# Optimization experiments

Measured on AMD Instinct MI355X. Metric: run time of the kernel, lower is better.

Reference implementation:

```python
import jax, jax.numpy as jnp
import numpy as np

B, L, A, S, H, K, M = 2048, 2, 4, 128, 256, 16, 131072


def _norm(x):
    # normalize_location: project onto unit sphere (last dim)
    return x / jnp.linalg.norm(x, axis=-1, keepdims=True)


def _mlp(x, W1, b1, W2, b2):
    return jax.nn.relu(x @ W1 + b1) @ W2 + b2


def _localizer_dist(loc, act, W1, b1, W2, b2, V1, c1, V2, c2, vs_logits):
    mean = _mlp(jnp.concatenate([loc, act], axis=1), W1, b1, W2, b2)
    sd = jnp.exp(_mlp(mean, V1, c1, V2, c2))
    sd = jnp.exp(vs_logits) * sd + 1e-6  # vs_logits has shape [L-1]==[1], broadcasts
    return mean, sd


def setup_inputs():
    key = jax.random.key(0)
    ks = jax.random.split(key, 12)
    return {
        'sensory': jax.random.normal(ks[0], (B, S)),
        'last_location': jax.random.normal(ks[1], (B, L)),
        'action': jax.random.normal(ks[2], (B, A)),
        'heading': jax.random.normal(ks[3], (B, A)),
        'mem_locations': jax.random.normal(ks[4], (M, L)),
        'mem_sensory': jax.random.normal(ks[5], (M, S)),
        'W1': jax.random.normal(ks[6], (L + A, H)) * 0.1,
        'b1': jnp.zeros((H,)),
        'W2': jax.random.normal(ks[7], (H, L)) * 0.1,
        'b2': jnp.zeros((L,)),
        'V1': jax.random.normal(ks[8], (L, H)) * 0.1,
        'c1': jnp.zeros((H,)),
        'V2': jax.random.normal(ks[9], (H, L)) * 0.1,
        'c2': jnp.zeros((L,)),
        'vs_logits': jnp.zeros((L - 1,)),
        'mem_valid_count': 8,
        'write_ptr': 1000,
    }


def reference(sensory, last_location, action, heading, mem_locations, mem_sensory,
              W1, b1, W2, b2, V1, c1, V2, c2, vs_logits, mem_valid_count, write_ptr):
    neg_inf = jnp.asarray(-jnp.inf, sensory.dtype)
    # --- memory.search: cosine-sim KNN over stored sensory keys ---
    q = _norm(sensory)                              # [B,S]
    keys = _norm(mem_sensory)                       # [M,S]
    scores_all = q @ keys.T                         # [B,M] big retrieval matmul
    valid = jnp.arange(M) < mem_valid_count         # [M]
    scores_all = jnp.where(valid[None, :], scores_all, neg_inf)
    scores, idx = jax.lax.top_k(scores_all, K)      # [B,K]
    location_guesses = mem_locations[idx]           # gather: [B,K,L]
    found = jnp.full((B,), min(mem_valid_count, K))
    # --- localizer: sample next agent location ---
    noise1 = jax.random.normal(jax.random.key(1), (B, L))
    noise2 = jax.random.normal(jax.random.key(2), (B, L))
    mean1, sd1 = _localizer_dist(last_location, action, W1, b1, W2, b2, V1, c1, V2, c2, vs_logits)
    next_location = mean1 + noise1 * sd1
    nl_lp = (-0.5 * (((next_location - mean1) / sd1) ** 2).sum(-1).mean()
             - jnp.log(sd1).sum(-1).mean())
    mean2, sd2 = _localizer_dist(next_location, heading, W1, b1, W2, b2, V1, c1, V2, c2, vs_logits)
    invalid_guess_mask = jnp.arange(K)[None, :] >= found[:, None]   # [B,K]
    ignore = found == 0                                             # [B]
    # --- select_location: masked similarity softmax over guesses ---
    # NOTE: torch `a.where(cond, b)` == where(cond, a, b); arg order preserved faithfully.
    matches = jnp.einsum('bkl,bl->bk', _norm(location_guesses), _norm(mean2))
    matches = jnp.where(invalid_guess_mask, matches, neg_inf)
    w = jax.nn.softmax(matches, axis=-1)
    integrated = jnp.einsum('bk,bkl->bl', w, location_guesses)
    too_far = jnp.linalg.norm(-0.5 * ((integrated - mean2) / sd2), axis=-1) > 2.0
    expected = mean2 + noise2 * sd2
    cond = too_far[:, None] | ignore[:, None] | jnp.isnan(integrated)
    obj_location = jnp.where(cond, integrated, expected)
    obj_lp = (-0.5 * (((obj_location - mean2) / sd2) ** 2).sum(-1).mean()
              - jnp.log(sd2).sum(-1).mean())
    # --- memory.write: scatter into ring buffer ---
    pos = (write_ptr + jnp.arange(B)) % M
    new_mem_loc = mem_locations.at[pos].set(obj_location)
    new_mem_sens = mem_sensory.at[pos].set(sensory)
    return next_location, nl_lp + obj_lp, new_mem_loc, new_mem_sens
```

## Files before the change

### kernel.cpp

```cpp
#include <hip/hip_runtime.h>
#include <stdint.h>

namespace {

constexpr int Bn = 2048;
constexpr int Kn = 16;
constexpr int Mn = 131072;

constexpr int O_NEXT   = 0;
constexpr int O_SCALAR = Bn * 2;
constexpr int O_LOC    = O_SCALAR + 1;
constexpr int O_SENS   = O_LOC + Mn * 2;

constexpr int NCOMPB = 512;
constexpr int NCOPY  = 2048;

constexpr int SENS_N = Mn * 128;
constexpr uint32_t RMASK = Mn - 1;
constexpr int NGI  = SENS_N / 4;
constexpr int TOTU = NGI + Mn;

typedef float f32x4   __attribute__((ext_vector_type(4)));
typedef float f32x4_u __attribute__((ext_vector_type(4), aligned(4)));

__device__ __forceinline__ uint32_t rotl32(uint32_t v, int d) {
  return (v << d) | (v >> (32 - d));
}
__device__ __forceinline__ void tfround(uint32_t& x0, uint32_t& x1, int r) {
  x0 += x1; x1 = rotl32(x1, r); x1 ^= x0;
}
__device__ __forceinline__ void threefry2x32(uint32_t k0, uint32_t k1,
                                             uint32_t c0, uint32_t c1,
                                             uint32_t& o0, uint32_t& o1) {
  const uint32_t ks2 = k0 ^ k1 ^ 0x1BD11BDAu;
  uint32_t x0 = c0 + k0, x1 = c1 + k1;
  tfround(x0, x1, 13); tfround(x0, x1, 15); tfround(x0, x1, 26); tfround(x0, x1, 6);
  x0 += k1;  x1 += ks2 + 1u;
  tfround(x0, x1, 17); tfround(x0, x1, 29); tfround(x0, x1, 16); tfround(x0, x1, 24);
  x0 += ks2; x1 += k0 + 2u;
  tfround(x0, x1, 13); tfround(x0, x1, 15); tfround(x0, x1, 26); tfround(x0, x1, 6);
  x0 += k0;  x1 += k1 + 3u;
  tfround(x0, x1, 17); tfround(x0, x1, 29); tfround(x0, x1, 16); tfround(x0, x1, 24);
  x0 += k1;  x1 += ks2 + 4u;
  tfround(x0, x1, 13); tfround(x0, x1, 15); tfround(x0, x1, 26); tfround(x0, x1, 6);
  o0 = x0 + ks2;
  o1 = x1 + k0 + 5u;
}

__device__ __forceinline__ float erfinv_xla(float x) {
  float w = -log1pf(-x * x);
  float p;
  if (w < 5.0f) {
    w -= 2.5f;
    p = 2.81022636e-08f;
    p = fmaf(p, w, 3.43273939e-07f);
    p = fmaf(p, w, -3.5233877e-06f);
    p = fmaf(p, w, -4.39150654e-06f);
    p = fmaf(p, w, 0.00021858087f);
    p = fmaf(p, w, -0.00125372503f);
    p = fmaf(p, w, -0.00417768164f);
    p = fmaf(p, w, 0.246640727f);
    p = fmaf(p, w, 1.50140941f);
  } else {
    w = sqrtf(w) - 3.0f;
    p = -0.000200214257f;
    p = fmaf(p, w, 0.000100950558f);
    p = fmaf(p, w, 0.00134934322f);
    p = fmaf(p, w, -0.00367342844f);
    p = fmaf(p, w, 0.00573950773f);
    p = fmaf(p, w, -0.0076224613f);
    p = fmaf(p, w, 0.00943887047f);
    p = fmaf(p, w, 1.00167406f);
    p = fmaf(p, w, 2.83297682f);
  }
  return p * x;
}
__device__ __forceinline__ float bits_to_normal(uint32_t bits) {
  const float lo = __int_as_float(0xBF7FFFFF);
  float f = __uint_as_float((bits >> 9) | 0x3F800000u) - 1.0f;
  float u = fmaxf(lo, f * 2.0f + lo);
  return 1.41421356237f * erfinv_xla(u);
}
__device__ __forceinline__ float noise_part(uint32_t key_lo, uint32_t i) {
  uint32_t o0, o1;
  threefry2x32(0u, key_lo, 0u, i, o0, o1);
  return bits_to_normal(o0 ^ o1);
}

__device__ __forceinline__ float wave_sum(float v) {
#pragma unroll
  for (int off = 32; off > 0; off >>= 1) v += __shfl_xor(v, off);
  return v;
}

__device__ __forceinline__ void localizer_wave(
    int lane,
    float x0, float x1, float x2, float x3, float x4, float x5,
    const float* __restrict__ W1, const float* __restrict__ b1,
    const float* __restrict__ W2, const float* __restrict__ b2,
    const float* __restrict__ V1, const float* __restrict__ c1,
    const float* __restrict__ V2, const float* __restrict__ c2,
    float vs_exp,
    float& m0, float& m1, float& sd0, float& sd1) {
  const int h = lane << 2;
  const float4 bb = *(const float4*)(b1 + h);
  const float4 w0 = *(const float4*)(W1 + h);
  const float4 w1 = *(const float4*)(W1 + 256 + h);
  const float4 w2 = *(const float4*)(W1 + 512 + h);
  const float4 w3 = *(const float4*)(W1 + 768 + h);
  const float4 w4 = *(const float4*)(W1 + 1024 + h);
  const float4 w5 = *(const float4*)(W1 + 1280 + h);
  float t0 = bb.x, t1 = bb.y, t2 = bb.z, t3 = bb.w;
  t0 = fmaf(x0, w0.x, t0); t1 = fmaf(x0, w0.y, t1); t2 = fmaf(x0, w0.z, t2); t3 = fmaf(x0, w0.w, t3);
  t0 = fmaf(x1, w1.x, t0); t1 = fmaf(x1, w1.y, t1); t2 = fmaf(x1, w1.z, t2); t3 = fmaf(x1, w1.w, t3);
  t0 = fmaf(x2, w2.x, t0); t1 = fmaf(x2, w2.y, t1); t2 = fmaf(x2, w2.z, t2); t3 = fmaf(x2, w2.w, t3);
  t0 = fmaf(x3, w3.x, t0); t1 = fmaf(x3, w3.y, t1); t2 = fmaf(x3, w3.z, t2); t3 = fmaf(x3, w3.w, t3);
  t0 = fmaf(x4, w4.x, t0); t1 = fmaf(x4, w4.y, t1); t2 = fmaf(x4, w4.z, t2); t3 = fmaf(x4, w4.w, t3);
  t0 = fmaf(x5, w5.x, t0); t1 = fmaf(x5, w5.y, t1); t2 = fmaf(x5, w5.z, t2); t3 = fmaf(x5, w5.w, t3);
  t0 = fmaxf(t0, 0.f); t1 = fmaxf(t1, 0.f); t2 = fmaxf(t2, 0.f); t3 = fmaxf(t3, 0.f);
  const float4 u0 = *(const float4*)(W2 + 2 * h);
  const float4 u1 = *(const float4*)(W2 + 2 * h + 4);
  float pa0 = t0 * u0.x; float pa1 = t0 * u0.y;
  pa0 = fmaf(t1, u0.z, pa0); pa1 = fmaf(t1, u0.w, pa1);
  pa0 = fmaf(t2, u1.x, pa0); pa1 = fmaf(t2, u1.y, pa1);
  pa0 = fmaf(t3, u1.z, pa0); pa1 = fmaf(t3, u1.w, pa1);
  m0 = wave_sum(pa0) + b2[0];
  m1 = wave_sum(pa1) + b2[1];

  const float4 cc = *(const float4*)(c1 + h);
  const float4 v0 = *(const float4*)(V1 + h);
  const float4 v1 = *(const float4*)(V1 + 256 + h);
  float s0 = cc.x, s1 = cc.y, s2 = cc.z, s3 = cc.w;
  s0 = fmaf(m0, v0.x, s0); s1 = fmaf(m0, v0.y, s1); s2 = fmaf(m0, v0.z, s2); s3 = fmaf(m0, v0.w, s3);
  s0 = fmaf(m1, v1.x, s0); s1 = fmaf(m1, v1.y, s1); s2 = fmaf(m1, v1.z, s2); s3 = fmaf(m1, v1.w, s3);
  s0 = fmaxf(s0, 0.f); s1 = fmaxf(s1, 0.f); s2 = fmaxf(s2, 0.f); s3 = fmaxf(s3, 0.f);
  const float4 q0 = *(const float4*)(V2 + 2 * h);
  const float4 q1 = *(const float4*)(V2 + 2 * h + 4);
  float ps0 = s0 * q0.x; float ps1 = s0 * q0.y;
  ps0 = fmaf(s1, q0.z, ps0); ps1 = fmaf(s1, q0.w, ps1);
  ps0 = fmaf(s2, q1.x, ps0); ps1 = fmaf(s2, q1.y, ps1);
  ps0 = fmaf(s3, q1.z, ps0); ps1 = fmaf(s3, q1.w, ps1);
  const float sv0 = wave_sum(ps0) + c2[0];
  const float sv1 = wave_sum(ps1) + c2[1];
  sd0 = fmaf(vs_exp, expf(sv0), 1e-6f);
  sd1 = fmaf(vs_exp, expf(sv1), 1e-6f);
}

__global__ __launch_bounds__(256) void fused_kernel(
    const float* __restrict__ sensory, const float* __restrict__ last_location,
    const float* __restrict__ action, const float* __restrict__ heading,
    const float* __restrict__ mem_locations, const float* __restrict__ mem_sensory,
    const float* __restrict__ W1, const float* __restrict__ b1,
    const float* __restrict__ W2, const float* __restrict__ b2,
    const float* __restrict__ V1, const float* __restrict__ c1,
    const float* __restrict__ V2, const float* __restrict__ c2,
    const float* __restrict__ vs_logits,
    const int* __restrict__ mvc_p, const int* __restrict__ wp_p,
    float* __restrict__ out, float* __restrict__ ws) {
  const int mvc = *mvc_p;
  const uint32_t wpm = (uint32_t)(*wp_p) & RMASK;

  if (blockIdx.x >= NCOMPB) {
    const int stride = NCOPY * 256;
    for (int u = (int)(blockIdx.x - NCOMPB) * 256 + (int)threadIdx.x;
         u < TOTU; u += stride) {
      if (u < NGI) {
        const uint32_t r  = (uint32_t)u >> 5;
        const uint32_t bb = (r - wpm) & RMASK;
        const int e = 4 * u;
        const float* src = (bb < Bn) ? (sensory + ((bb << 7) | (e & 127)))
                                     : (mem_sensory + e);
        const f32x4 q = *(const f32x4*)src;
        __builtin_nontemporal_store(q, (f32x4_u*)(out + O_SENS + e));
      } else {
        const uint32_t r = (uint32_t)(u - NGI);
        const uint32_t bb = (r - wpm) & RMASK;
        if (bb >= Bn) {
          const float2 v = *(const float2*)(mem_locations + 2 * r);
          out[O_LOC + 2 * r]     = v.x;
          out[O_LOC + 2 * r + 1] = v.y;
        }
      }
    }
  } else {
    __shared__ float redc[4][4];
    const int cb = blockIdx.x;
    const int wid = threadIdx.x >> 6;
    const int lane = threadIdx.x & 63;
    const int b = cb * 4 + wid;

    const uint32_t nk = 1u + ((lane >> 1) & 1u);
    const uint32_t ni = (uint32_t)(2 * b) + (lane & 1u);
    const float nv = noise_part(nk, ni);
    const float n1a = __shfl(nv, 0);
    const float n1b = __shfl(nv, 1);
    const float n2a = __shfl(nv, 2);
    const float n2b = __shfl(nv, 3);

    const float vs_exp = expf(vs_logits[0]);
    const float l0 = last_location[2 * b], l1 = last_location[2 * b + 1];
    const float a0 = action[4 * b],     a1 = action[4 * b + 1];
    const float a2 = action[4 * b + 2], a3 = action[4 * b + 3];
    const float h0 = heading[4 * b],     h1 = heading[4 * b + 1];
    const float h2 = heading[4 * b + 2], h3 = heading[4 * b + 3];

    float m10, m11, sd10, sd11;
    localizer_wave(lane, l0, l1, a0, a1, a2, a3, W1, b1, W2, b2, V1, c1, V2, c2,
                   vs_exp, m10, m11, sd10, sd11);
    const float nl0 = m10 + n1a * sd10;
    const float nl1 = m11 + n1b * sd11;
    if (lane == 0) *(float2*)(out + 2 * b) = make_float2(nl0, nl1);

    const float d0 = (nl0 - m10) / sd10;
    const float d1 = (nl1 - m11) / sd11;
    const float v_sq1 = d0 * d0 + d1 * d1;
    const float v_lg1 = logf(sd10) + logf(sd11);

    float m20, m21, sd20, sd21;
    localizer_wave(lane, nl0, nl1, h0, h1, h2, h3, W1, b1, W2, b2, V1, c1, V2, c2,
                   vs_exp, m20, m21, sd20, sd21);

    const int found = (mvc < Kn) ? mvc : Kn;
    const bool ignore = (found == 0);
    const float NEG_INF = -__builtin_huge_valf();

    const float qn = sqrtf(m20 * m20 + m21 * m21);
    const float q0 = m20 / qn, q1 = m21 / qn;

    float mk[Kn];
#pragma unroll
    for (int k = 0; k < Kn; ++k) {
      if (k >= found) {
        const float g0 = mem_locations[2 * k], g1 = mem_locations[2 * k + 1];
        const float gn = sqrtf(g0 * g0 + g1 * g1);
        mk[k] = (g0 / gn) * q0 + (g1 / gn) * q1;
      } else {
        mk[k] = NEG_INF;
      }
    }
    float mmax = NEG_INF;
#pragma unroll
    for (int k = 0; k < Kn; ++k) mmax = fmaxf(mmax, mk[k]);
    float wsum = 0.f;
#pragma unroll
    for (int k = 0; k < Kn; ++k) {
      mk[k] = expf(mk[k] - mmax);
      wsum += mk[k];
    }
    float i0 = 0.f, i1 = 0.f;
#pragma unroll
    for (int k = 0; k < Kn; ++k) {
      const float wn = mk[k] / wsum;
      i0 = fmaf(wn, mem_locations[2 * k], i0);
      i1 = fmaf(wn, mem_locations[2 * k + 1], i1);
    }

    const float z0 = (i0 - m20) / sd20, z1 = (i1 - m21) / sd21;
    const float hz0 = -0.5f * z0, hz1 = -0.5f * z1;
    const bool too_far = sqrtf(hz0 * hz0 + hz1 * hz1) > 2.0f;
    const float e0 = m20 + n2a * sd20;
    const float e1 = m21 + n2b * sd21;
    const bool c0 = too_far || ignore || __builtin_isnan(i0);
    const bool c1 = too_far || ignore || __builtin_isnan(i1);
    const float o0 = c0 ? i0 : e0;
    const float o1 = c1 ? i1 : e1;

    if (lane == 0) {
      const uint32_t row = (wpm + (uint32_t)b) & RMASK;
      out[O_LOC + 2 * row]     = o0;
      out[O_LOC + 2 * row + 1] = o1;
    }

    const float zo0 = (o0 - m20) / sd20, zo1 = (o1 - m21) / sd21;
    const float v_sq2 = zo0 * zo0 + zo1 * zo1;
    const float v_lg2 = logf(sd20) + logf(sd21);

    if (lane == 0) {
      redc[wid][0] = v_sq1; redc[wid][1] = v_lg1;
      redc[wid][2] = v_sq2; redc[wid][3] = v_lg2;
    }
    __syncthreads();
    if (threadIdx.x == 0) {
      float s0 = 0.f, s1 = 0.f, s2 = 0.f, s3 = 0.f;
#pragma unroll
      for (int w = 0; w < 4; ++w) {
        s0 += redc[w][0]; s1 += redc[w][1]; s2 += redc[w][2]; s3 += redc[w][3];
      }
      ws[4 * cb + 0] = s0; ws[4 * cb + 1] = s1;
      ws[4 * cb + 2] = s2; ws[4 * cb + 3] = s3;
    }
  }
}

__global__ void finalize_kernel(const float* __restrict__ ws, float* __restrict__ out) {
  const int lane = threadIdx.x;
  float s0 = 0.f, s1 = 0.f, s2 = 0.f, s3 = 0.f;
  for (int i = lane; i < NCOMPB; i += 64) {
    s0 += ws[4 * i + 0]; s1 += ws[4 * i + 1];
    s2 += ws[4 * i + 2]; s3 += ws[4 * i + 3];
  }
#pragma unroll
  for (int off = 32; off > 0; off >>= 1) {
    s0 += __shfl_xor(s0, off); s1 += __shfl_xor(s1, off);
    s2 += __shfl_xor(s2, off); s3 += __shfl_xor(s3, off);
  }
  if (lane == 0) {
    const float invB = 1.0f / (float)Bn;
    const float nl_lp  = -0.5f * (s0 * invB) - (s1 * invB);
    const float obj_lp = -0.5f * (s2 * invB) - (s3 * invB);
    out[O_SCALAR] = nl_lp + obj_lp;
  }
}

}

extern "C" void kernel_launch(void* const* d_in, const int* in_sizes, int n_in,
                              void* d_out, int out_size, void* d_ws, size_t ws_size,
                              hipStream_t stream) {
  const float* sensory       = (const float*)d_in[0];
  const float* last_location = (const float*)d_in[1];
  const float* action        = (const float*)d_in[2];
  const float* heading       = (const float*)d_in[3];
  const float* mem_locations = (const float*)d_in[4];
  const float* mem_sensory   = (const float*)d_in[5];
  const float* W1 = (const float*)d_in[6];
  const float* b1 = (const float*)d_in[7];
  const float* W2 = (const float*)d_in[8];
  const float* b2 = (const float*)d_in[9];
  const float* V1 = (const float*)d_in[10];
  const float* c1 = (const float*)d_in[11];
  const float* V2 = (const float*)d_in[12];
  const float* c2 = (const float*)d_in[13];
  const float* vs = (const float*)d_in[14];
  const int* mvc  = (const int*)d_in[15];
  const int* wp   = (const int*)d_in[16];
  float* out = (float*)d_out;
  float* ws  = (float*)d_ws;

  fused_kernel<<<dim3(NCOMPB + NCOPY), dim3(256), 0, stream>>>(
      sensory, last_location, action, heading, mem_locations, mem_sensory,
      W1, b1, W2, b2, V1, c1, V2, c2, vs, mvc, wp, out, ws);
  finalize_kernel<<<dim3(1), dim3(64), 0, stream>>>(ws, out);
}
```

Measured before the change: 30.43 us.

## Unroll ring-buffer copy to fixed 64B chunks and move location copy to compute blocks

The copy blocks no longer run a grid-stride loop. Each thread now copies exactly two 64-byte chunks of the sensory ring buffer, issuing all eight 16-byte loads before any stores to raise memory-level parallelism. The mem_locations copy moves into the compute blocks: its load is issued early and its store is placed after the first localizer, so it overlaps with compute. This depends on the copy grid size matching the buffer exactly (2048 blocks × 256 threads × 2 × 16 floats = M×128) and on the compute blocks covering all M rows (512 × 256 = M), so the fixed sizes become hard-wired assumptions.

```diff
diff --git a/kernel.cpp b/kernel.cpp
--- a/kernel.cpp
+++ b/kernel.cpp
@@ -17,8 +17,7 @@
 
 constexpr int SENS_N = Mn * 128;
 constexpr uint32_t RMASK = Mn - 1;
-constexpr int NGI  = SENS_N / 4;
-constexpr int TOTU = NGI + Mn;
+constexpr int CTHREADS = NCOPY * 256;
 
 typedef float f32x4   __attribute__((ext_vector_type(4)));
 typedef float f32x4_u __attribute__((ext_vector_type(4), aligned(4)));
@@ -146,6 +145,15 @@
   sd1 = fmaf(vs_exp, expf(sv1), 1e-6f);
 }
 
+__device__ __forceinline__ const float* quad_src(
+    uint32_t q, uint32_t wpm,
+    const float* __restrict__ sensory, const float* __restrict__ mem_sensory) {
+  const uint32_t r  = q >> 3;
+  const uint32_t bb = (r - wpm) & RMASK;
+  const uint32_t col = (q & 7u) << 4;
+  return (bb < Bn) ? (sensory + ((bb << 7) | col)) : (mem_sensory + 16 * q);
+}
+
 __global__ __launch_bounds__(256) void fused_kernel(
     const float* __restrict__ sensory, const float* __restrict__ last_location,
     const float* __restrict__ action, const float* __restrict__ heading,
@@ -161,33 +169,43 @@
   const uint32_t wpm = (uint32_t)(*wp_p) & RMASK;
 
   if (blockIdx.x >= NCOMPB) {
-    const int stride = NCOPY * 256;
-    for (int u = (int)(blockIdx.x - NCOMPB) * 256 + (int)threadIdx.x;
-         u < TOTU; u += stride) {
-      if (u < NGI) {
-        const uint32_t r  = (uint32_t)u >> 5;
-        const uint32_t bb = (r - wpm) & RMASK;
-        const int e = 4 * u;
-        const float* src = (bb < Bn) ? (sensory + ((bb << 7) | (e & 127)))
-                                     : (mem_sensory + e);
-        const f32x4 q = *(const f32x4*)src;
-        __builtin_nontemporal_store(q, (f32x4_u*)(out + O_SENS + e));
-      } else {
-        const uint32_t r = (uint32_t)(u - NGI);
-        const uint32_t bb = (r - wpm) & RMASK;
-        if (bb >= Bn) {
-          const float2 v = *(const float2*)(mem_locations + 2 * r);
-          out[O_LOC + 2 * r]     = v.x;
-          out[O_LOC + 2 * r + 1] = v.y;
-        }
-      }
-    }
+    const uint32_t T  = (uint32_t)(blockIdx.x - NCOMPB) * 256 + threadIdx.x;
+    const uint32_t q0 = T;
+    const uint32_t q1 = T + (uint32_t)CTHREADS;
+
+    const float* s0 = quad_src(q0, wpm, sensory, mem_sensory);
+    const float* s1 = quad_src(q1, wpm, sensory, mem_sensory);
+
+    const f32x4 a0 = *(const f32x4*)(s0 + 0);
+    const f32x4 a1 = *(const f32x4*)(s0 + 4);
+    const f32x4 a2 = *(const f32x4*)(s0 + 8);
+    const f32x4 a3 = *(const f32x4*)(s0 + 12);
+    const f32x4 b0 = *(const f32x4*)(s1 + 0);
+    const f32x4 b1v = *(const f32x4*)(s1 + 4);
+    const f32x4 b2v = *(const f32x4*)(s1 + 8);
+    const f32x4 b3 = *(const f32x4*)(s1 + 12);
+
+    float* d0 = out + O_SENS + 16 * q0;
+    float* d1 = out + O_SENS + 16 * q1;
+    __builtin_nontemporal_store(a0, (f32x4_u*)(d0 + 0));
+    __builtin_nontemporal_store(a1, (f32x4_u*)(d0 + 4));
+    __builtin_nontemporal_store(a2, (f32x4_u*)(d0 + 8));
+    __builtin_nontemporal_store(a3, (f32x4_u*)(d0 + 12));
+    __builtin_nontemporal_store(b0, (f32x4_u*)(d1 + 0));
+    __builtin_nontemporal_store(b1v, (f32x4_u*)(d1 + 4));
+    __builtin_nontemporal_store(b2v, (f32x4_u*)(d1 + 8));
+    __builtin_nontemporal_store(b3, (f32x4_u*)(d1 + 12));
   } else {
     __shared__ float redc[4][4];
     const int cb = blockIdx.x;
     const int wid = threadIdx.x >> 6;
     const int lane = threadIdx.x & 63;
     const int b = cb * 4 + wid;
+
+    const uint32_t lr  = (uint32_t)(cb * 256) + threadIdx.x;
+    const uint32_t lbb = (lr - wpm) & RMASK;
+    float2 lv = make_float2(0.f, 0.f);
+    if (lbb >= Bn) lv = *(const float2*)(mem_locations + 2 * lr);
 
     const uint32_t nk = 1u + ((lane >> 1) & 1u);
     const uint32_t ni = (uint32_t)(2 * b) + (lane & 1u);
@@ -215,6 +233,11 @@
     const float d1 = (nl1 - m11) / sd11;
     const float v_sq1 = d0 * d0 + d1 * d1;
     const float v_lg1 = logf(sd10) + logf(sd11);
+
+    if (lbb >= Bn) {
+      out[O_LOC + 2 * lr]     = lv.x;
+      out[O_LOC + 2 * lr + 1] = lv.y;
+    }
 
     float m20, m21, sd20, sd21;
     localizer_wave(lane, nl0, nl1, h0, h1, h2, h3, W1, b1, W2, b2, V1, c1, V2, c2,
```

After: 93.86 us (median of 5 runs). +208.4%, slower.

## Batch sensory copy loads per thread and move location copy into compute blocks

Applied to the files above, without the earlier changes.

The copy blocks now issue eight independent 16-byte loads per thread before their nontemporal stores, replacing a strided loop with a per-iteration branch, so more memory requests are in flight. The location ring-buffer copy is moved into the compute blocks: each thread loads one row early and stores it after the first localizer pass, hiding the load latency behind compute. In exchange, the compute blocks gain extra memory traffic and register pressure, and the copy geometry is hardcoded to the exact element count.

```diff
diff --git a/kernel.cpp b/kernel.cpp
--- a/kernel.cpp
+++ b/kernel.cpp
@@ -17,8 +17,8 @@
 
 constexpr int SENS_N = Mn * 128;
 constexpr uint32_t RMASK = Mn - 1;
-constexpr int NGI  = SENS_N / 4;
-constexpr int TOTU = NGI + Mn;
+constexpr int CTHREADS = NCOPY * 256;
+constexpr int NSLOT = 8;
 
 typedef float f32x4   __attribute__((ext_vector_type(4)));
 typedef float f32x4_u __attribute__((ext_vector_type(4), aligned(4)));
@@ -161,26 +161,22 @@
   const uint32_t wpm = (uint32_t)(*wp_p) & RMASK;
 
   if (blockIdx.x >= NCOMPB) {
-    const int stride = NCOPY * 256;
-    for (int u = (int)(blockIdx.x - NCOMPB) * 256 + (int)threadIdx.x;
-         u < TOTU; u += stride) {
-      if (u < NGI) {
-        const uint32_t r  = (uint32_t)u >> 5;
-        const uint32_t bb = (r - wpm) & RMASK;
-        const int e = 4 * u;
-        const float* src = (bb < Bn) ? (sensory + ((bb << 7) | (e & 127)))
-                                     : (mem_sensory + e);
-        const f32x4 q = *(const f32x4*)src;
-        __builtin_nontemporal_store(q, (f32x4_u*)(out + O_SENS + e));
-      } else {
-        const uint32_t r = (uint32_t)(u - NGI);
-        const uint32_t bb = (r - wpm) & RMASK;
-        if (bb >= Bn) {
-          const float2 v = *(const float2*)(mem_locations + 2 * r);
-          out[O_LOC + 2 * r]     = v.x;
-          out[O_LOC + 2 * r + 1] = v.y;
-        }
-      }
+    const uint32_t T = (uint32_t)(blockIdx.x - NCOMPB) * 256 + threadIdx.x;
+    f32x4 v[NSLOT];
+#pragma unroll
+    for (int k = 0; k < NSLOT; ++k) {
+      const uint32_t g  = (uint32_t)k * (uint32_t)CTHREADS + T;
+      const uint32_t r  = g >> 5;
+      const uint32_t bb = (r - wpm) & RMASK;
+      const uint32_t col = (g & 31u) << 2;
+      const float* src = (bb < Bn) ? (sensory + ((bb << 7) | col))
+                                   : (mem_sensory + 4u * g);
+      v[k] = *(const f32x4*)src;
+    }
+#pragma unroll
+    for (int k = 0; k < NSLOT; ++k) {
+      const uint32_t g = (uint32_t)k * (uint32_t)CTHREADS + T;
+      __builtin_nontemporal_store(v[k], (f32x4_u*)(out + O_SENS + 4u * g));
     }
   } else {
     __shared__ float redc[4][4];
@@ -188,6 +184,11 @@
     const int wid = threadIdx.x >> 6;
     const int lane = threadIdx.x & 63;
     const int b = cb * 4 + wid;
+
+    const uint32_t lr  = (uint32_t)(cb * 256) + threadIdx.x;
+    const uint32_t lbb = (lr - wpm) & RMASK;
+    float2 lv = make_float2(0.f, 0.f);
+    if (lbb >= Bn) lv = *(const float2*)(mem_locations + 2 * lr);
 
     const uint32_t nk = 1u + ((lane >> 1) & 1u);
     const uint32_t ni = (uint32_t)(2 * b) + (lane & 1u);
@@ -215,6 +216,11 @@
     const float d1 = (nl1 - m11) / sd11;
     const float v_sq1 = d0 * d0 + d1 * d1;
     const float v_lg1 = logf(sd10) + logf(sd11);
+
+    if (lbb >= Bn) {
+      out[O_LOC + 2 * lr]     = lv.x;
+      out[O_LOC + 2 * lr + 1] = lv.y;
+    }
 
     float m20, m21, sd20, sd21;
     localizer_wave(lane, nl0, nl1, h0, h1, h2, h3, W1, b1, W2, b2, V1, c1, V2, c2,
```

After: 33.46 us. 1.1x slower.
